# Performance work log

Measured on AMD Instinct MI355X. Metric: run time of the kernel, lower is better.

The kernel has to match this reference:

```python
import jax, jax.numpy as jnp
import numpy as np

LOG2 = 0.6931471805599453  # shifted_softplus(x) = softplus(x) - log(2)
NUM_MOL = 20_000  # static maxm for segment reduction


def ssp(x):
    return jax.nn.softplus(x) - LOG2


def setup_inputs() -> dict:
    key = jax.random.key(0)
    ks = jax.random.split(key, 5)
    N, D, H, E, M = 1_000_000, 128, 64, 4, NUM_MOL
    x = jax.random.normal(ks[0], (N, D), dtype=jnp.float32)
    zidx = jax.random.randint(ks[1], (N,), 0, E, dtype=jnp.int32)
    idx_m = jnp.sort(jax.random.randint(ks[2], (N,), 0, M, dtype=jnp.int32))
    # stacked per-element pyramidal MLP params: D -> D//2 -> 1
    W1 = jax.random.normal(ks[3], (E, D, H), dtype=jnp.float32) * (1.0 / np.sqrt(D))
    b1 = jnp.zeros((E, H), dtype=jnp.float32)
    W2 = jax.random.normal(ks[4], (E, H, 1), dtype=jnp.float32) * (1.0 / np.sqrt(H))
    b2 = jnp.zeros((E, 1), dtype=jnp.float32)
    return dict(x=x, zidx=zidx, idx_m=idx_m, W1=W1, b1=b1, W2=W2, b2=b2)


def reference(x, zidx, idx_m, W1, b1, W2, b2):
    # ElementwiseMLP: run each element's 2-layer MLP, select per atom by element.
    E = W1.shape[0]
    yi = jnp.zeros((x.shape[0], W2.shape[-1]), dtype=x.dtype)  # [N, n_out]
    for e in range(E):  # small fixed element set
        h = ssp(x @ W1[e] + b1[e])            # [N, H]
        ye = h @ W2[e] + b2[e]                # [N, n_out]
        yi = yi + jnp.where((zidx == e)[:, None], ye, jnp.zeros((), dtype=x.dtype))
    # aggregation_mode == 'sum': index_add per molecule
    y = jax.ops.segment_sum(yi, idx_m, num_segments=NUM_MOL)  # [M, n_out]
    return jnp.squeeze(y, -1)  # [M]
```

## Files before the change

kernel.cpp:

```cpp
#include <hip/hip_runtime.h>

typedef _Float16 half8 __attribute__((ext_vector_type(8)));
typedef float f32x4 __attribute__((ext_vector_type(4)));

#define WS_COUNT(e)  ((e) * 32)
#define WS_AOFF(e)   (128 + (e))
#define WS_FILL(e)   (136 + (e))
#define WS_CUR(e)    (160 + (e) * 32)
#define WS_PERM      512

__global__ void k_count(const int* __restrict__ zidx, int N, int* __restrict__ ws,
                        const float* __restrict__ W1, _Float16* __restrict__ w1h) {
  __shared__ int lh[4];
  if (threadIdx.x < 4) lh[threadIdx.x] = 0;
  __syncthreads();
  const int i = blockIdx.x * 256 + threadIdx.x;
  const int z = (i < N) ? zidx[i] : -1;
  const int lane = threadIdx.x & 63;
#pragma unroll
  for (int e = 0; e < 4; ++e) {
    unsigned long long m = __ballot(z == e);
    if (lane == 0 && m) atomicAdd(&lh[e], __popcll(m));
  }
  if (blockIdx.x < 16) {
    const int cg = blockIdx.x * 256 + threadIdx.x;
    const int e = cg >> 10, ch = cg & 1023;
    const int kt = ch >> 8, nt = (ch >> 6) & 3, l2 = ch & 63;
    const int h = nt * 16 + (l2 & 15);
    const int d0 = kt * 32 + (l2 >> 4) * 8;
    const float* w1e = W1 + (size_t)e * 8192;
    half8 hv;
#pragma unroll
    for (int j = 0; j < 8; ++j) hv[j] = (_Float16)w1e[(d0 + j) * 64 + h];
    *(half8*)&w1h[(size_t)cg * 8] = hv;
  }
  __syncthreads();
  if (threadIdx.x < 4 && lh[threadIdx.x])
    atomicAdd(&ws[WS_COUNT(threadIdx.x)], lh[threadIdx.x]);
}

__global__ void k_offsets(int* __restrict__ ws) {
  if (threadIdx.x != 0) return;
  int off = 0;
#pragma unroll
  for (int e = 0; e < 4; ++e) {
    int c = ws[WS_COUNT(e)];
    ws[WS_AOFF(e)] = off;
    ws[WS_FILL(e)] = off + c;
    ws[WS_CUR(e)] = off;
    off += (c + 255) & ~255;
  }
  ws[WS_AOFF(4)] = off;
}

__global__ void k_scatter(const int* __restrict__ zidx, int N, int* __restrict__ ws) {
  __shared__ int wcnt[4][4];
  __shared__ int wbase[4][4];
  const int tid = threadIdx.x;
  const int lane = tid & 63;
  const int wave = tid >> 6;
  const int i = blockIdx.x * 256 + tid;
  const int z = (i < N) ? zidx[i] : -1;
  const unsigned long long m0 = __ballot(z == 0);
  const unsigned long long m1 = __ballot(z == 1);
  const unsigned long long m2 = __ballot(z == 2);
  const unsigned long long m3 = __ballot(z == 3);
  if (lane == 0) {
    wcnt[wave][0] = __popcll(m0);
    wcnt[wave][1] = __popcll(m1);
    wcnt[wave][2] = __popcll(m2);
    wcnt[wave][3] = __popcll(m3);
  }
  __syncthreads();
  if (tid < 4) {
    const int e = tid;
    const int c0 = wcnt[0][e], c1 = wcnt[1][e], c2 = wcnt[2][e], c3 = wcnt[3][e];
    const int base = atomicAdd(&ws[WS_CUR(e)], c0 + c1 + c2 + c3);
    wbase[0][e] = base;
    wbase[1][e] = base + c0;
    wbase[2][e] = base + c0 + c1;
    wbase[3][e] = base + c0 + c1 + c2;
  }
  __syncthreads();
  if (z >= 0) {
    const unsigned long long below = (1ull << lane) - 1ull;
    int r, b;
    if (z == 0)      { r = __popcll(m0 & below); b = wbase[wave][0]; }
    else if (z == 1) { r = __popcll(m1 & below); b = wbase[wave][1]; }
    else if (z == 2) { r = __popcll(m2 & below); b = wbase[wave][2]; }
    else             { r = __popcll(m3 & below); b = wbase[wave][3]; }
    ws[WS_PERM + b + r] = i;
  }
}

__global__ __launch_bounds__(256, 4)
void elemental_sorted16(const float* __restrict__ x,
                        const int* __restrict__ idx_m,
                        const _Float16* __restrict__ w1h,
                        const float* __restrict__ b1,
                        const float* __restrict__ W2,
                        const float* __restrict__ b2,
                        const int* __restrict__ ws,
                        float* __restrict__ y) {
  __shared__ _Float16 w1t[8192];

  const int bstart = blockIdx.x * 64;
  if (bstart >= ws[WS_AOFF(4)]) return;
  int e = 0;
  if (bstart >= ws[WS_AOFF(1)]) e = 1;
  if (bstart >= ws[WS_AOFF(2)]) e = 2;
  if (bstart >= ws[WS_AOFF(3)]) e = 3;
  const int fillE = ws[WS_FILL(e)];

  const int tid = threadIdx.x;
  const half8* src = (const half8*)w1h + (size_t)e * 1024;
#pragma unroll
  for (int it = 0; it < 4; ++it) {
    const int kk = it * 256 + tid;
    *(half8*)&w1t[kk * 8] = src[kk];
  }
  __syncthreads();

  const int lane = tid & 63;
  const int wave = tid >> 6;
  const int c = lane & 15;
  const int q = lane >> 4;
  const int pos = bstart + wave * 16 + c;
  const int ap = (pos < fillE) ? ws[WS_PERM + pos] : -1;
  const int iv = (ap >= 0) ? idx_m[ap] : 0;

  const f32x4* rp = (const f32x4*)(x + (long)(ap < 0 ? 0 : ap) * 128);
  half8 af[4];
#pragma unroll
  for (int kt = 0; kt < 4; ++kt) {
    f32x4 u0 = rp[kt * 8 + q * 2];
    f32x4 u1 = rp[kt * 8 + q * 2 + 1];
    half8 a;
    a[0] = (_Float16)u0[0]; a[1] = (_Float16)u0[1];
    a[2] = (_Float16)u0[2]; a[3] = (_Float16)u0[3];
    a[4] = (_Float16)u1[0]; a[5] = (_Float16)u1[1];
    a[6] = (_Float16)u1[2]; a[7] = (_Float16)u1[3];
    af[kt] = a;
  }

  f32x4 acc[4];
#pragma unroll
  for (int nt = 0; nt < 4; ++nt) acc[nt] = (f32x4){0.f, 0.f, 0.f, 0.f};
#pragma unroll
  for (int kt = 0; kt < 4; ++kt)
#pragma unroll
    for (int nt = 0; nt < 4; ++nt) {
      half8 bf = *(const half8*)&w1t[((kt * 4 + nt) * 64 + lane) * 8];
      acc[nt] = __builtin_amdgcn_mfma_f32_16x16x32_f16(af[kt], bf, acc[nt], 0, 0, 0);
    }

  float b1v[4], w2v[4];
#pragma unroll
  for (int nt = 0; nt < 4; ++nt) {
    b1v[nt] = b1[e * 64 + nt * 16 + c];
    w2v[nt] = W2[e * 64 + nt * 16 + c];
  }
  const float b2e = b2[e];
#pragma unroll
  for (int i = 0; i < 4; ++i) {
    float s = 0.0f;
#pragma unroll
    for (int nt = 0; nt < 4; ++nt) {
      float tv = acc[nt][i] + b1v[nt];
      float hsp = __logf(1.0f + __expf(tv)) - 0.69314718056f;
      s = fmaf(hsp, w2v[nt], s);
    }
    s += __shfl_xor(s, 1);
    s += __shfl_xor(s, 2);
    s += __shfl_xor(s, 4);
    s += __shfl_xor(s, 8);
    const int slot = q * 4 + i;
    const int av = __shfl(ap, slot);
    const int im = __shfl(iv, slot);
    if (c == 0 && av >= 0)
      atomicAdd(&y[im], s + b2e);
  }
}

#define LDSROW_OLD 136

__global__ __launch_bounds__(256, 2)
void elemental_atomwise_kernel(const float* __restrict__ x,
                               const int* __restrict__ zidx,
                               const int* __restrict__ idx_m,
                               const float* __restrict__ W1,
                               const float* __restrict__ b1,
                               const float* __restrict__ W2,
                               const float* __restrict__ b2,
                               float* __restrict__ y,
                               int N) {
  extern __shared__ _Float16 w1t[];
#pragma unroll
  for (int it = 0; it < 32; ++it) {
    int idx4 = threadIdx.x + it * 256;
    f32x4 v = ((const f32x4*)W1)[idx4];
    int lin = idx4 << 2;
    int d = (lin >> 6) & 127;
    int ee = lin >> 13;
    int h = lin & 63;
    int n = ee * 64 + h;
#pragma unroll
    for (int j = 0; j < 4; ++j)
      w1t[(n + j) * LDSROW_OLD + d] = (_Float16)v[j];
  }
  __syncthreads();

  const int lane = threadIdx.x & 63;
  const int wave = threadIdx.x >> 6;
  const int c = lane & 15;
  const int q = lane >> 4;
  const long tile = (long)blockIdx.x * 4 + wave;
  const long base = tile * 64;
  if (base >= N) return;

  int ameta = (base + lane < N) ? (int)(base + lane) : (N - 1);
  const int zvec = zidx[ameta];
  const int ivec = idx_m[ameta];

  half8 af[4][4];
#pragma unroll
  for (int mt = 0; mt < 4; ++mt) {
    long row = base + mt * 16 + c;
    if (row >= N) row = N - 1;
    const f32x4* rp = (const f32x4*)(x + row * 128);
#pragma unroll
    for (int kt = 0; kt < 4; ++kt) {
      f32x4 u0 = rp[kt * 8 + q * 2];
      f32x4 u1 = rp[kt * 8 + q * 2 + 1];
      half8 a;
      a[0] = (_Float16)u0[0]; a[1] = (_Float16)u0[1];
      a[2] = (_Float16)u0[2]; a[3] = (_Float16)u0[3];
      a[4] = (_Float16)u1[0]; a[5] = (_Float16)u1[1];
      a[6] = (_Float16)u1[2]; a[7] = (_Float16)u1[3];
      af[mt][kt] = a;
    }
  }

#pragma unroll
  for (int e = 0; e < 4; ++e) {
    f32x4 acc[4][4];
#pragma unroll
    for (int mt = 0; mt < 4; ++mt)
#pragma unroll
      for (int nt = 0; nt < 4; ++nt)
        acc[mt][nt] = (f32x4){0.f, 0.f, 0.f, 0.f};

#pragma unroll
    for (int kt = 0; kt < 4; ++kt) {
#pragma unroll
      for (int nt = 0; nt < 4; ++nt) {
        half8 bf = *(const half8*)&w1t[(e * 64 + nt * 16 + c) * LDSROW_OLD + kt * 32 + q * 8];
#pragma unroll
        for (int mt = 0; mt < 4; ++mt)
          acc[mt][nt] = __builtin_amdgcn_mfma_f32_16x16x32_f16(af[mt][kt], bf, acc[mt][nt], 0, 0, 0);
      }
    }

    float b1v[4], w2v[4];
#pragma unroll
    for (int nt = 0; nt < 4; ++nt) {
      b1v[nt] = b1[e * 64 + nt * 16 + c];
      w2v[nt] = W2[e * 64 + nt * 16 + c];
    }
    const float b2e = b2[e];
#pragma unroll
    for (int mt = 0; mt < 4; ++mt) {
#pragma unroll
      for (int i = 0; i < 4; ++i) {
        float s = 0.0f;
#pragma unroll
        for (int nt = 0; nt < 4; ++nt) {
          float tv = acc[mt][nt][i] + b1v[nt];
          float hsp = __logf(1.0f + __expf(tv)) - 0.69314718056f;
          s = fmaf(hsp, w2v[nt], s);
        }
        s += __shfl_xor(s, 1);
        s += __shfl_xor(s, 2);
        s += __shfl_xor(s, 4);
        s += __shfl_xor(s, 8);
        int mloc = mt * 16 + q * 4 + i;
        int zm = __shfl(zvec, mloc);
        int im = __shfl(ivec, mloc);
        if (c == 0 && zm == e && base + mloc < N)
          atomicAdd(&y[im], s + b2e);
      }
    }
  }
}

extern "C" void kernel_launch(void* const* d_in, const int* in_sizes, int n_in,
                              void* d_out, int out_size, void* d_ws, size_t ws_size,
                              hipStream_t stream) {
  const float* x = (const float*)d_in[0];
  const int* zidx = (const int*)d_in[1];
  const int* idx_m = (const int*)d_in[2];
  const float* W1 = (const float*)d_in[3];
  const float* b1 = (const float*)d_in[4];
  const float* W2 = (const float*)d_in[5];
  const float* b2 = (const float*)d_in[6];
  float* y = (float*)d_out;

  const int N = in_sizes[0] / 128;

  hipMemsetAsync(d_out, 0, (size_t)out_size * sizeof(float), stream);

  const int w1h_off = (512 + N + 1024 + 3) & ~3;
  const size_t ws_need = (size_t)w1h_off * sizeof(int) + 65536;
  if (ws_size >= ws_need) {
    int* ws = (int*)d_ws;
    _Float16* w1h = (_Float16*)(ws + w1h_off);
    hipMemsetAsync(d_ws, 0, 1024, stream);
    const int nb = (N + 255) / 256;
    const int nbc = nb < 16 ? 16 : nb;
    k_count<<<nbc, 256, 0, stream>>>(zidx, N, ws, W1, w1h);
    k_offsets<<<1, 64, 0, stream>>>(ws);
    k_scatter<<<nb, 256, 0, stream>>>(zidx, N, ws);
    const int nb64 = (N + 1020 + 63) / 64;
    elemental_sorted16<<<nb64, 256, 0, stream>>>(x, idx_m, w1h, b1, W2, b2, ws, y);
  } else {
    const int tiles = (N + 63) / 64;
    const int blocks = (tiles + 3) / 4;
    const size_t lds_bytes = 256 * LDSROW_OLD * sizeof(_Float16);
    elemental_atomwise_kernel<<<blocks, 256, lds_bytes, stream>>>(
        x, zidx, idx_m, W1, b1, W2, b2, y, N);
  }
}
```

Measured before the change: 768.5 us.

## Process 512 atoms per block with double-buffered loads and segmented atomic reduction

The main kernel now handles eight 64-atom groups per block, double-buffering the x row loads against MFMA compute. This amortizes the W1 LDS staging across more work and hides global load latency. Per-group outputs are combined with a wave-level segmented scan over sorted idx_m, so only one atomic is issued per molecule run instead of one per atom. The offsets kernel is removed: offsets are recomputed inline from the counts, and count/scatter each process 1024 atoms per block, which cuts launches and per-block overhead at the cost of higher register pressure.

```diff
diff --git a/kernel.cpp b/kernel.cpp
--- a/kernel.cpp
+++ b/kernel.cpp
@@ -4,8 +4,6 @@
 typedef float f32x4 __attribute__((ext_vector_type(4)));
 
 #define WS_COUNT(e)  ((e) * 32)
-#define WS_AOFF(e)   (128 + (e))
-#define WS_FILL(e)   (136 + (e))
 #define WS_CUR(e)    (160 + (e) * 32)
 #define WS_PERM      512
 
@@ -13,15 +11,6 @@
                         const float* __restrict__ W1, _Float16* __restrict__ w1h) {
   __shared__ int lh[4];
   if (threadIdx.x < 4) lh[threadIdx.x] = 0;
-  __syncthreads();
-  const int i = blockIdx.x * 256 + threadIdx.x;
-  const int z = (i < N) ? zidx[i] : -1;
-  const int lane = threadIdx.x & 63;
-#pragma unroll
-  for (int e = 0; e < 4; ++e) {
-    unsigned long long m = __ballot(z == e);
-    if (lane == 0 && m) atomicAdd(&lh[e], __popcll(m));
-  }
   if (blockIdx.x < 16) {
     const int cg = blockIdx.x * 256 + threadIdx.x;
     const int e = cg >> 10, ch = cg & 1023;
@@ -35,82 +24,178 @@
     *(half8*)&w1h[(size_t)cg * 8] = hv;
   }
   __syncthreads();
+  const int lane = threadIdx.x & 63;
+  const int base = blockIdx.x * 1024;
+  int pc[4] = {0, 0, 0, 0};
+#pragma unroll
+  for (int it = 0; it < 4; ++it) {
+    const int i = base + it * 256 + threadIdx.x;
+    const int z = (i < N) ? zidx[i] : -1;
+#pragma unroll
+    for (int e = 0; e < 4; ++e) {
+      unsigned long long m = __ballot(z == e);
+      if (lane == 0) pc[e] += __popcll(m);
+    }
+  }
+  if (lane == 0) {
+#pragma unroll
+    for (int e = 0; e < 4; ++e)
+      if (pc[e]) atomicAdd(&lh[e], pc[e]);
+  }
+  __syncthreads();
   if (threadIdx.x < 4 && lh[threadIdx.x])
     atomicAdd(&ws[WS_COUNT(threadIdx.x)], lh[threadIdx.x]);
 }
 
-__global__ void k_offsets(int* __restrict__ ws) {
-  if (threadIdx.x != 0) return;
-  int off = 0;
-#pragma unroll
-  for (int e = 0; e < 4; ++e) {
-    int c = ws[WS_COUNT(e)];
-    ws[WS_AOFF(e)] = off;
-    ws[WS_FILL(e)] = off + c;
-    ws[WS_CUR(e)] = off;
-    off += (c + 255) & ~255;
-  }
-  ws[WS_AOFF(4)] = off;
-}
-
 __global__ void k_scatter(const int* __restrict__ zidx, int N, int* __restrict__ ws) {
-  __shared__ int wcnt[4][4];
-  __shared__ int wbase[4][4];
-  const int tid = threadIdx.x;
-  const int lane = tid & 63;
-  const int wave = tid >> 6;
-  const int i = blockIdx.x * 256 + tid;
-  const int z = (i < N) ? zidx[i] : -1;
-  const unsigned long long m0 = __ballot(z == 0);
-  const unsigned long long m1 = __ballot(z == 1);
-  const unsigned long long m2 = __ballot(z == 2);
-  const unsigned long long m3 = __ballot(z == 3);
-  if (lane == 0) {
-    wcnt[wave][0] = __popcll(m0);
-    wcnt[wave][1] = __popcll(m1);
-    wcnt[wave][2] = __popcll(m2);
-    wcnt[wave][3] = __popcll(m3);
+  __shared__ int cnts[4][4][4];
+  __shared__ int pb[4][4][4];
+  const int tid = threadIdx.x, lane = tid & 63, wave = tid >> 6;
+  const int base = blockIdx.x * 1024;
+  int zz[4];
+#pragma unroll
+  for (int it = 0; it < 4; ++it) {
+    const int i = base + it * 256 + tid;
+    zz[it] = (i < N) ? zidx[i] : -1;
+#pragma unroll
+    for (int e = 0; e < 4; ++e) {
+      unsigned long long m = __ballot(zz[it] == e);
+      if (lane == 0) cnts[it][wave][e] = __popcll(m);
+    }
   }
   __syncthreads();
   if (tid < 4) {
     const int e = tid;
-    const int c0 = wcnt[0][e], c1 = wcnt[1][e], c2 = wcnt[2][e], c3 = wcnt[3][e];
-    const int base = atomicAdd(&ws[WS_CUR(e)], c0 + c1 + c2 + c3);
-    wbase[0][e] = base;
-    wbase[1][e] = base + c0;
-    wbase[2][e] = base + c0 + c1;
-    wbase[3][e] = base + c0 + c1 + c2;
-  }
-  __syncthreads();
-  if (z >= 0) {
-    const unsigned long long below = (1ull << lane) - 1ull;
-    int r, b;
-    if (z == 0)      { r = __popcll(m0 & below); b = wbase[wave][0]; }
-    else if (z == 1) { r = __popcll(m1 & below); b = wbase[wave][1]; }
-    else if (z == 2) { r = __popcll(m2 & below); b = wbase[wave][2]; }
-    else             { r = __popcll(m3 & below); b = wbase[wave][3]; }
-    ws[WS_PERM + b + r] = i;
-  }
-}
+    int off = 0, aoffe = 0;
+#pragma unroll
+    for (int k = 0; k < 4; ++k) {
+      int ck = ws[WS_COUNT(k)];
+      if (k == e) aoffe = off;
+      off += (ck + 511) & ~511;
+    }
+    int tot = 0;
+#pragma unroll
+    for (int it = 0; it < 4; ++it)
+#pragma unroll
+      for (int w = 0; w < 4; ++w) tot += cnts[it][w][e];
+    const int cur = atomicAdd(&ws[WS_CUR(e)], tot);
+    int run = aoffe + cur;
+#pragma unroll
+    for (int it = 0; it < 4; ++it)
+#pragma unroll
+      for (int w = 0; w < 4; ++w) { pb[it][w][e] = run; run += cnts[it][w][e]; }
+  }
+  __syncthreads();
+  const unsigned long long below = (1ull << lane) - 1ull;
+#pragma unroll
+  for (int it = 0; it < 4; ++it) {
+    const int z = zz[it];
+    const unsigned long long m0 = __ballot(z == 0);
+    const unsigned long long m1 = __ballot(z == 1);
+    const unsigned long long m2 = __ballot(z == 2);
+    const unsigned long long m3 = __ballot(z == 3);
+    if (z >= 0) {
+      const unsigned long long me = (z == 0) ? m0 : (z == 1) ? m1 : (z == 2) ? m2 : m3;
+      const int r = __popcll(me & below);
+      ws[WS_PERM + pb[it][wave][z] + r] = base + it * 256 + tid;
+    }
+  }
+}
+
+#define LOADF(dst, g_) do {                                                     \
+    const int ap_ = apv[g_];                                                    \
+    const f32x4* rp_ = (const f32x4*)(x + (long)(ap_ < 0 ? 0 : ap_) * 128);     \
+    _Pragma("unroll")                                                           \
+    for (int kt = 0; kt < 4; ++kt) {                                            \
+      f32x4 u0 = rp_[kt * 8 + q * 2];                                           \
+      f32x4 u1 = rp_[kt * 8 + q * 2 + 1];                                       \
+      half8 a;                                                                  \
+      a[0] = (_Float16)u0[0]; a[1] = (_Float16)u0[1];                           \
+      a[2] = (_Float16)u0[2]; a[3] = (_Float16)u0[3];                           \
+      a[4] = (_Float16)u1[0]; a[5] = (_Float16)u1[1];                           \
+      a[6] = (_Float16)u1[2]; a[7] = (_Float16)u1[3];                           \
+      dst[kt] = a;                                                              \
+    }                                                                           \
+  } while (0)
+
+#define COMPUTE(g_, af_) do {                                                   \
+    f32x4 acc[4];                                                               \
+    _Pragma("unroll")                                                           \
+    for (int nt = 0; nt < 4; ++nt) acc[nt] = (f32x4){0.f, 0.f, 0.f, 0.f};       \
+    _Pragma("unroll")                                                           \
+    for (int kt = 0; kt < 4; ++kt)                                              \
+      _Pragma("unroll")                                                         \
+      for (int nt = 0; nt < 4; ++nt) {                                          \
+        half8 bf = *(const half8*)&w1t[((kt * 4 + nt) * 64 + lane) * 8];        \
+        acc[nt] = __builtin_amdgcn_mfma_f32_16x16x32_f16(af_[kt], bf, acc[nt], 0, 0, 0); \
+      }                                                                         \
+    float sv[4];                                                                \
+    _Pragma("unroll")                                                           \
+    for (int i = 0; i < 4; ++i) {                                               \
+      float s = 0.0f;                                                           \
+      _Pragma("unroll")                                                         \
+      for (int nt = 0; nt < 4; ++nt) {                                          \
+        float tv = acc[nt][i] + b1v[nt];                                        \
+        float hsp = __logf(1.0f + __expf(tv)) - 0.69314718056f;                 \
+        s = fmaf(hsp, w2v[nt], s);                                              \
+      }                                                                         \
+      s += __shfl_xor(s, 1);                                                    \
+      s += __shfl_xor(s, 2);                                                    \
+      s += __shfl_xor(s, 4);                                                    \
+      s += __shfl_xor(s, 8);                                                    \
+      sv[i] = s;                                                                \
+    }                                                                           \
+        \
+    const int srcl = (lane >> 2) << 4;                                          \
+    float t0 = __shfl(sv[0], srcl);                                             \
+    float t1 = __shfl(sv[1], srcl);                                             \
+    float t2 = __shfl(sv[2], srcl);                                             \
+    float t3 = __shfl(sv[3], srcl);                                             \
+    const int r3 = lane & 3;                                                    \
+    float val = (r3 == 0) ? t0 : (r3 == 1) ? t1 : (r3 == 2) ? t2 : t3;          \
+    const int apl = apv[g_];                                                    \
+    const int ivl = ivv[g_];                                                    \
+    val = (apl >= 0) ? val + b2e : 0.0f;                                        \
+    const int ivp = __shfl_up(ivl, 1);                                          \
+    const int head = (lane == 0) || (ivl != ivp);                               \
+    int flg = head;                                                             \
+    float v = val;                                                              \
+    _Pragma("unroll")                                                           \
+    for (int d = 1; d < 16; d <<= 1) {                                          \
+      float v2 = __shfl_up(v, d);                                               \
+      int f2 = __shfl_up(flg, d);                                               \
+      if (lane >= d && !flg) v += v2;                                           \
+      if (lane >= d) flg |= f2;                                                 \
+    }                                                                           \
+    const int nh = __shfl_down(head, 1);                                        \
+    if (lane < 16 && ((lane == 15) || nh)) atomicAdd(&y[ivl], v);               \
+  } while (0)
 
 __global__ __launch_bounds__(256, 4)
-void elemental_sorted16(const float* __restrict__ x,
-                        const int* __restrict__ idx_m,
-                        const _Float16* __restrict__ w1h,
-                        const float* __restrict__ b1,
-                        const float* __restrict__ W2,
-                        const float* __restrict__ b2,
-                        const int* __restrict__ ws,
-                        float* __restrict__ y) {
+void elemental_main(const float* __restrict__ x,
+                    const int* __restrict__ idx_m,
+                    const _Float16* __restrict__ w1h,
+                    const float* __restrict__ b1,
+                    const float* __restrict__ W2,
+                    const float* __restrict__ b2,
+                    const int* __restrict__ ws,
+                    float* __restrict__ y) {
   __shared__ _Float16 w1t[8192];
 
-  const int bstart = blockIdx.x * 64;
-  if (bstart >= ws[WS_AOFF(4)]) return;
-  int e = 0;
-  if (bstart >= ws[WS_AOFF(1)]) e = 1;
-  if (bstart >= ws[WS_AOFF(2)]) e = 2;
-  if (bstart >= ws[WS_AOFF(3)]) e = 3;
-  const int fillE = ws[WS_FILL(e)];
+  int cw[4];
+#pragma unroll
+  for (int k = 0; k < 4; ++k) cw[k] = ws[WS_COUNT(k)];
+  const int aoff1 = (cw[0] + 511) & ~511;
+  const int aoff2 = aoff1 + ((cw[1] + 511) & ~511);
+  const int aoff3 = aoff2 + ((cw[2] + 511) & ~511);
+  const int aoff4 = aoff3 + ((cw[3] + 511) & ~511);
+  const int bstart = blockIdx.x * 512;
+  if (bstart >= aoff4) return;
+  int e = 0, ao = 0;
+  if (bstart >= aoff1) { e = 1; ao = aoff1; }
+  if (bstart >= aoff2) { e = 2; ao = aoff2; }
+  if (bstart >= aoff3) { e = 3; ao = aoff3; }
+  const int fillE = ao + cw[e];
 
   const int tid = threadIdx.x;
   const half8* src = (const half8*)w1h + (size_t)e * 1024;
@@ -119,40 +204,11 @@
     const int kk = it * 256 + tid;
     *(half8*)&w1t[kk * 8] = src[kk];
   }
-  __syncthreads();
 
   const int lane = tid & 63;
   const int wave = tid >> 6;
   const int c = lane & 15;
   const int q = lane >> 4;
-  const int pos = bstart + wave * 16 + c;
-  const int ap = (pos < fillE) ? ws[WS_PERM + pos] : -1;
-  const int iv = (ap >= 0) ? idx_m[ap] : 0;
-
-  const f32x4* rp = (const f32x4*)(x + (long)(ap < 0 ? 0 : ap) * 128);
-  half8 af[4];
-#pragma unroll
-  for (int kt = 0; kt < 4; ++kt) {
-    f32x4 u0 = rp[kt * 8 + q * 2];
-    f32x4 u1 = rp[kt * 8 + q * 2 + 1];
-    half8 a;
-    a[0] = (_Float16)u0[0]; a[1] = (_Float16)u0[1];
-    a[2] = (_Float16)u0[2]; a[3] = (_Float16)u0[3];
-    a[4] = (_Float16)u1[0]; a[5] = (_Float16)u1[1];
-    a[6] = (_Float16)u1[2]; a[7] = (_Float16)u1[3];
-    af[kt] = a;
-  }
-
-  f32x4 acc[4];
-#pragma unroll
-  for (int nt = 0; nt < 4; ++nt) acc[nt] = (f32x4){0.f, 0.f, 0.f, 0.f};
-#pragma unroll
-  for (int kt = 0; kt < 4; ++kt)
-#pragma unroll
-    for (int nt = 0; nt < 4; ++nt) {
-      half8 bf = *(const half8*)&w1t[((kt * 4 + nt) * 64 + lane) * 8];
-      acc[nt] = __builtin_amdgcn_mfma_f32_16x16x32_f16(af[kt], bf, acc[nt], 0, 0, 0);
-    }
 
   float b1v[4], w2v[4];
 #pragma unroll
@@ -161,25 +217,37 @@
     w2v[nt] = W2[e * 64 + nt * 16 + c];
   }
   const float b2e = b2[e];
-#pragma unroll
-  for (int i = 0; i < 4; ++i) {
-    float s = 0.0f;
-#pragma unroll
-    for (int nt = 0; nt < 4; ++nt) {
-      float tv = acc[nt][i] + b1v[nt];
-      float hsp = __logf(1.0f + __expf(tv)) - 0.69314718056f;
-      s = fmaf(hsp, w2v[nt], s);
-    }
-    s += __shfl_xor(s, 1);
-    s += __shfl_xor(s, 2);
-    s += __shfl_xor(s, 4);
-    s += __shfl_xor(s, 8);
-    const int slot = q * 4 + i;
-    const int av = __shfl(ap, slot);
-    const int im = __shfl(iv, slot);
-    if (c == 0 && av >= 0)
-      atomicAdd(&y[im], s + b2e);
-  }
+
+  int apv[8], ivv[8];
+  const int pbase = bstart + wave * 16 + c;
+#pragma unroll
+  for (int g = 0; g < 8; ++g) {
+    const int pos = pbase + g * 64;
+    apv[g] = (pos < fillE) ? ws[WS_PERM + pos] : -1;
+  }
+#pragma unroll
+  for (int g = 0; g < 8; ++g)
+    ivv[g] = (apv[g] >= 0) ? idx_m[apv[g]] : 0;
+
+  __syncthreads();
+
+  half8 afA[4], afB[4];
+  LOADF(afA, 0);
+  LOADF(afB, 1);
+  COMPUTE(0, afA);
+  LOADF(afA, 2);
+  COMPUTE(1, afB);
+  LOADF(afB, 3);
+  COMPUTE(2, afA);
+  LOADF(afA, 4);
+  COMPUTE(3, afB);
+  LOADF(afB, 5);
+  COMPUTE(4, afA);
+  LOADF(afA, 6);
+  COMPUTE(5, afB);
+  LOADF(afB, 7);
+  COMPUTE(6, afA);
+  COMPUTE(7, afB);
 }
 
 #define LDSROW_OLD 136
@@ -309,19 +377,18 @@
 
   hipMemsetAsync(d_out, 0, (size_t)out_size * sizeof(float), stream);
 
-  const int w1h_off = (512 + N + 1024 + 3) & ~3;
+  const int w1h_off = (512 + N + 2048 + 3) & ~3;
   const size_t ws_need = (size_t)w1h_off * sizeof(int) + 65536;
   if (ws_size >= ws_need) {
     int* ws = (int*)d_ws;
     _Float16* w1h = (_Float16*)(ws + w1h_off);
-    hipMemsetAsync(d_ws, 0, 1024, stream);
-    const int nb = (N + 255) / 256;
+    hipMemsetAsync(d_ws, 0, 2048, stream);
+    const int nb = (N + 1023) / 1024;
     const int nbc = nb < 16 ? 16 : nb;
     k_count<<<nbc, 256, 0, stream>>>(zidx, N, ws, W1, w1h);
-    k_offsets<<<1, 64, 0, stream>>>(ws);
     k_scatter<<<nb, 256, 0, stream>>>(zidx, N, ws);
-    const int nb64 = (N + 1020 + 63) / 64;
-    elemental_sorted16<<<nb64, 256, 0, stream>>>(x, idx_m, w1h, b1, W2, b2, ws, y);
+    const int mb = (N + 2555) / 512;
+    elemental_main<<<mb, 256, 0, stream>>>(x, idx_m, w1h, b1, W2, b2, ws, y);
   } else {
     const int tiles = (N + 63) / 64;
     const int blocks = (tiles + 3) / 4;
```

Measured after the change: 703.9 us. 8.4% less time.
